# Performance work log

Measured on AMD Instinct MI355X. Metric: run time of the kernel, lower is better.

The kernel has to match this reference:

```python
import jax, jax.numpy as jnp
import numpy as np

N, C, T, H, W = 2, 512, 8, 28, 28
THW = T * H * W
BN_EPS = 1e-5


def conv1x1(x, Wt, b):
    # pointwise channel mixing, equivalent to 1x1 Conv2d/Conv3d on (N,C,T,H,W)
    return jnp.einsum('oc,ncthw->nothw', Wt, x) + b[None, :, None, None, None]


def setup_inputs() -> dict:
    key = jax.random.key(0)
    ks = jax.random.split(key, 8)
    s = 1.0 / np.sqrt(C)
    x = jax.random.normal(ks[0], (N, C, T, H, W), dtype=jnp.float32)
    mask = jax.random.uniform(ks[1], (N, C, T, H, W), dtype=jnp.float32)
    Wh = jax.random.normal(ks[2], (C, C), dtype=jnp.float32) * s
    Wg = jax.random.normal(ks[3], (C, C), dtype=jnp.float32) * s
    Wm = jax.random.normal(ks[4], (C, C), dtype=jnp.float32) * s
    Wz = jax.random.normal(ks[5], (C, C), dtype=jnp.float32) * s  # kaiming-like
    bh = jnp.zeros((C,), jnp.float32)
    bg = jnp.zeros((C,), jnp.float32)
    bm = jnp.zeros((C,), jnp.float32)
    bz = jnp.zeros((C,), jnp.float32)
    bn_w = jnp.ones((C,), jnp.float32)
    bn_b = jnp.zeros((C,), jnp.float32)
    gamma = jnp.float32(1.0)  # self.gamma (undefined in source __init__); learnable scalar
    return dict(x=x, mask=mask, Wh=Wh, bh=bh, Wg=Wg, bg=bg, Wm=Wm, bm=bm,
                Wz=Wz, bz=bz, bn_w=bn_w, bn_b=bn_b, gamma=gamma)


def reference(x, mask, Wh, bh, Wg, bg, Wm, bm, Wz, bz, bn_w, bn_b, gamma):
    n = x.shape[0]
    # proj_f = h(x) reshaped (N, THW, C); proj_g = g(x) (N, C, THW)
    ph_x = conv1x1(x, Wh, bh).reshape(n, C, THW)
    pg = conv1x1(x, Wg, bg).reshape(n, C, THW)
    # energy[n,t,s] = sum_c ph_x[n,c,t] * pg[n,c,s]  -> (N, THW, THW)
    energy = jnp.einsum('nct,ncs->nts', ph_x, pg)
    attention = jax.nn.softmax(energy, axis=-1)
    # proj_h uses self.h on mask (faithful to source)
    ph_m = conv1x1(mask, Wh, bh).reshape(n, C, THW)
    # bmm(proj_h, attention^T): [n,c,t] = sum_s ph_m[n,c,s] * attention[n,t,s]
    mask_energy = jnp.einsum('ncs,nts->nct', ph_m, attention)
    mask_atten = jax.nn.softmax(mask_energy, axis=-1)  # softmax over THW
    pm = conv1x1(x, Wm, bm)
    out = pm * mask_atten.reshape(n, C, T, H, W)
    # W_z: 1x1 Conv3d + BatchNorm3d (training-mode batch stats, weight=1, bias=0)
    wy = conv1x1(x, Wz, bz)
    mu = jnp.mean(wy, axis=(0, 2, 3, 4), keepdims=True)
    var = jnp.var(wy, axis=(0, 2, 3, 4), keepdims=True)
    wy = (wy - mu) * jax.lax.rsqrt(var + BN_EPS)
    wy = wy * bn_w[None, :, None, None, None] + bn_b[None, :, None, None, None]
    return gamma * out + wy
```

## Files before the change

kernel.cpp:

```cpp
#include <hip/hip_runtime.h>
#include <hip/hip_bf16.h>
#include <math.h>

#define NN 2
#define CC 512
#define PP 6272
#define TCHMAX 1664
#define NCHK 4
#define NJT 49
#define EM 64.0f
static const size_t PPC = (size_t)PP * CC;
static const size_t NCP = (size_t)NN * PPC;

typedef unsigned short ushortT;
typedef __attribute__((ext_vector_type(8))) short short8;
typedef __attribute__((ext_vector_type(4))) float f32x4;

#define WAITV(N) asm volatile("s_waitcnt vmcnt(" #N ")" ::: "memory")
#define BAR() __builtin_amdgcn_s_barrier()

__device__ __forceinline__ ushortT f2bf(float f) {
  __hip_bfloat16 h = __float2bfloat16(f);
  return *reinterpret_cast<ushortT*>(&h);
}
__device__ __forceinline__ float bf2f(ushortT u) {
  return __uint_as_float(((unsigned)u) << 16);
}

__device__ __forceinline__ void ld_g2l(const void* g, void* l) {
  __builtin_amdgcn_global_load_lds(
      (const __attribute__((address_space(1))) void*)g,
      (__attribute__((address_space(3))) void*)l, 16, 0, 0);
}

__device__ __forceinline__ int xcd_remap(int orig, int nwg) {
  const int q = nwg >> 3, r = nwg & 7;
  const int x = orig & 7, lo = orig >> 3;
  return (x < r) ? x * (q + 1) + lo : r * (q + 1) + (x - r) * q + lo;
}


__global__ __launch_bounds__(256) void k_prep(const float* __restrict__ x,
                                              const float* __restrict__ mask,
                                              const float* __restrict__ W0,
                                              const float* __restrict__ W1,
                                              const float* __restrict__ W2,
                                              const float* __restrict__ W3,
                                              ushortT* __restrict__ Wbf,
                                              ushortT* __restrict__ xT,
                                              ushortT* __restrict__ maskT) {
  __shared__ float T[32][33];
  const int tid = threadIdx.x;
  int b = blockIdx.x;
  if (b < 1024) {
    const int by = b >> 8, bx = b & 255;
    const float* src = (by == 0) ? W0 : (by == 1) ? W1 : (by == 2) ? W2 : W3;
    const int i = (bx * 256 + tid) * 4;
    float4 v = *(const float4*)&src[i];
    ushort4 o;
    o.x = f2bf(v.x); o.y = f2bf(v.y); o.z = f2bf(v.z); o.w = f2bf(v.w);
    *(ushort4*)&Wbf[(size_t)by * CC * CC + i] = o;
    return;
  }
  b -= 1024;
  const int bx = b % 196;
  const int by = (b / 196) & 15;
  const int zz = b / (196 * 16);
  const float* in = (zz < 2) ? x : mask;
  ushortT* out = (zz < 2) ? xT : maskT;
  const int p0 = bx * 32, c0 = by * 32;
  const int tx = tid & 31, ty = tid >> 5;
  const size_t nbi = (size_t)(zz & 1) * PPC;
#pragma unroll
  for (int i = 0; i < 4; ++i)
    T[ty + i * 8][tx] = in[nbi + (size_t)(c0 + ty + i * 8) * PP + p0 + tx];
  __syncthreads();
#pragma unroll
  for (int i = 0; i < 4; ++i) {
    int r = ty + i * 8;
    out[nbi + (size_t)(p0 + r) * CC + c0 + tx] = f2bf(T[tx][r]);
  }
}

__global__ __launch_bounds__(256, 2) void k_convs(
    const ushortT* __restrict__ xT, const ushortT* __restrict__ maskT,
    const ushortT* __restrict__ Whbf, const ushortT* __restrict__ Wgbf,
    const ushortT* __restrict__ Wmbf, const ushortT* __restrict__ Wzbf,
    const float* __restrict__ bh, const float* __restrict__ bg,
    const float* __restrict__ bm, const float* __restrict__ bz,
    ushortT* __restrict__ phxT, ushortT* __restrict__ pgT,
    ushortT* __restrict__ phmB, ushortT* __restrict__ pmB,
    ushortT* __restrict__ wzb) {
  __shared__ __align__(16) ushortT smem[36864];
  const int tid = threadIdx.x;
  const int l = tid & 63, w = tid >> 6;
  const int orig = blockIdx.x;
  const int wgid = (orig & 7) * 147 + (orig >> 3);
  const int zq = wgid / 196;
  const int within = wgid % 196;
  const int ctile = within & 3;
  const int ptile = within >> 2;
  const int wA = (w & 1) * 64, wB = (w >> 1) * 64;
  const int lr = l & 15, lk = l >> 4;
  const int r4 = (l >> 4) * 4;
  const int srow = l >> 2;
  const int sg8 = ((l & 3) ^ ((l >> 3) & 3)) * 8;
  const int rg16 = (lk ^ ((lr >> 1) & 3)) * 16;

  int offL[4], offR[4];
#pragma unroll
  for (int t = 0; t < 4; ++t) {
    offL[t] = (wA + t * 16 + lr) * 64 + rg16;
    offR[t] = (wB + t * 16 + lr) * 64 + rg16;
  }

  auto stage = [&](const ushortT* src, ushortT* dst) {
#pragma unroll
    for (int i = 0; i < 2; ++i)
      ld_g2l(src + (size_t)(w * 32 + i * 16 + srow) * CC + sg8,
             (char*)dst + (w * 2 + i) * 1024);
  };
  auto ldf = [&](const ushortT* base, const int* off, short8* f) {
#pragma unroll
    for (int t = 0; t < 4; ++t)
      f[t] = *(const short8*)((const char*)base + off[t]);
  };

  ushortT* Ca = smem;          ushortT* Na = smem + 4096;  ushortT* Za = smem + 8192;
  ushortT* Cb = smem + 12288;  ushortT* Nb = smem + 16384; ushortT* Zb = smem + 20480;
  ushortT* Cc = smem + 24576;  ushortT* Nc = smem + 28672; ushortT* Zc = smem + 32768;

  if (zq < 2) {
    const int zb = zq;
    const int p0 = ptile * 128, c0 = ctile * 128;
    const ushortT* Ax = xT + (size_t)zb * PPC + (size_t)p0 * CC;
    const ushortT* Bw1 = Whbf + (size_t)c0 * CC;
    const ushortT* Bw2 = Wgbf + (size_t)c0 * CC;
    ushortT* o1 = phxT + (size_t)zb * PPC;
    ushortT* o2 = pgT + (size_t)zb * PPC;
    f32x4 a1[4][4] = {}, a2[4][4] = {};
    stage(Ax, Ca); stage(Bw1, Cb); stage(Bw2, Cc);
    stage(Ax + 32, Na); stage(Bw1 + 32, Nb); stage(Bw2 + 32, Nc);
    WAITV(6); BAR();
    for (int t = 0; t < 16; ++t) {
      if (t < 14) {
        const int k = (t + 2) * 32;
        stage(Ax + k, Za); stage(Bw1 + k, Zb); stage(Bw2 + k, Zc);
      }
      short8 fp[4], fw[4];
      ldf(Ca, offL, fp);
      ldf(Cb, offR, fw);
      __builtin_amdgcn_s_setprio(1);
#pragma unroll
      for (int ss = 0; ss < 4; ++ss)
#pragma unroll
        for (int tt = 0; tt < 4; ++tt)
          a1[ss][tt] = __builtin_amdgcn_mfma_f32_16x16x32_bf16(fw[ss], fp[tt], a1[ss][tt], 0, 0, 0);
      __builtin_amdgcn_s_setprio(0);
      ldf(Cc, offR, fw);
      __builtin_amdgcn_s_setprio(1);
#pragma unroll
      for (int ss = 0; ss < 4; ++ss)
#pragma unroll
        for (int tt = 0; tt < 4; ++tt)
          a2[ss][tt] = __builtin_amdgcn_mfma_f32_16x16x32_bf16(fw[ss], fp[tt], a2[ss][tt], 0, 0, 0);
      __builtin_amdgcn_s_setprio(0);
      if (t < 14) { WAITV(6); } else { WAITV(0); }
      BAR();
      ushortT* tp;
      tp = Ca; Ca = Na; Na = Za; Za = tp;
      tp = Cb; Cb = Nb; Nb = Zb; Zb = tp;
      tp = Cc; Cc = Nc; Nc = Zc; Zc = tp;
    }
#pragma unroll
    for (int tt = 0; tt < 4; ++tt) {
      const size_t prow = (size_t)(p0 + wA + tt * 16 + lr) * CC;
#pragma unroll
      for (int ss = 0; ss < 4; ++ss) {
        const int co = c0 + wB + ss * 16 + r4;
        float4 b1v = *(const float4*)&bh[co];
        float4 b2v = *(const float4*)&bg[co];
        ushort4 v1, v2;
        v1.x = f2bf(a1[ss][tt][0] + b1v.x);
        v1.y = f2bf(a1[ss][tt][1] + b1v.y);
        v1.z = f2bf(a1[ss][tt][2] + b1v.z);
        v1.w = f2bf(a1[ss][tt][3] + b1v.w);
        v2.x = f2bf(a2[ss][tt][0] + b2v.x);
        v2.y = f2bf(a2[ss][tt][1] + b2v.y);
        v2.z = f2bf(a2[ss][tt][2] + b2v.z);
        v2.w = f2bf(a2[ss][tt][3] + b2v.w);
        *(ushort4*)&o1[prow + co] = v1;
        *(ushort4*)&o2[prow + co] = v2;
      }
    }
  } else if (zq < 4) {
    const int zb = zq - 2;
    const int s0 = ptile * 128, c0 = ctile * 128;
    const ushortT* Am = maskT + (size_t)zb * PPC + (size_t)s0 * CC;
    const ushortT* Bw = Whbf + (size_t)c0 * CC;
    ushortT* o = phmB + (size_t)zb * PPC;
    f32x4 a[4][4] = {};
    stage(Am, Ca); stage(Bw, Cb);
    stage(Am + 32, Na); stage(Bw + 32, Nb);
    WAITV(4); BAR();
    for (int t = 0; t < 16; ++t) {
      if (t < 14) {
        const int k = (t + 2) * 32;
        stage(Am + k, Za); stage(Bw + k, Zb);
      }
      short8 fs[4], fc[4];
      ldf(Ca, offL, fs);
      ldf(Cb, offR, fc);
      __builtin_amdgcn_s_setprio(1);
#pragma unroll
      for (int ss = 0; ss < 4; ++ss)
#pragma unroll
        for (int tt = 0; tt < 4; ++tt)
          a[ss][tt] = __builtin_amdgcn_mfma_f32_16x16x32_bf16(fs[ss], fc[tt], a[ss][tt], 0, 0, 0);
      __builtin_amdgcn_s_setprio(0);
      if (t < 14) { WAITV(4); } else { WAITV(0); }
      BAR();
      ushortT* tp;
      tp = Ca; Ca = Na; Na = Za; Za = tp;
      tp = Cb; Cb = Nb; Nb = Zb; Zb = tp;
    }
#pragma unroll
    for (int tt = 0; tt < 4; ++tt) {
      const int c = c0 + wB + tt * 16 + lr;
      const float bi = bh[c];
      const size_t crow = (size_t)c * PP;
#pragma unroll
      for (int ss = 0; ss < 4; ++ss) {
        ushort4 v;
        v.x = f2bf(a[ss][tt][0] + bi);
        v.y = f2bf(a[ss][tt][1] + bi);
        v.z = f2bf(a[ss][tt][2] + bi);
        v.w = f2bf(a[ss][tt][3] + bi);
        *(ushort4*)&o[crow + s0 + wA + ss * 16 + r4] = v;
      }
    }
  } else {
    const int zb = zq - 4;
    const int p0 = ptile * 128, c0 = ctile * 128;
    const ushortT* Ax = xT + (size_t)zb * PPC + (size_t)p0 * CC;
    const ushortT* Bw1 = Wmbf + (size_t)c0 * CC;
    const ushortT* Bw2 = Wzbf + (size_t)c0 * CC;
    ushortT* o1 = pmB + (size_t)zb * PPC;
    ushortT* o2 = wzb + (size_t)zb * PPC;
    f32x4 a1[4][4] = {}, a2[4][4] = {};
    stage(Ax, Ca); stage(Bw1, Cb); stage(Bw2, Cc);
    stage(Ax + 32, Na); stage(Bw1 + 32, Nb); stage(Bw2 + 32, Nc);
    WAITV(6); BAR();
    for (int t = 0; t < 16; ++t) {
      if (t < 14) {
        const int k = (t + 2) * 32;
        stage(Ax + k, Za); stage(Bw1 + k, Zb); stage(Bw2 + k, Zc);
      }
      short8 fx[4], fw[4];
      ldf(Ca, offL, fx);
      ldf(Cb, offR, fw);
      __builtin_amdgcn_s_setprio(1);
#pragma unroll
      for (int ss = 0; ss < 4; ++ss)
#pragma unroll
        for (int tt = 0; tt < 4; ++tt)
          a1[ss][tt] = __builtin_amdgcn_mfma_f32_16x16x32_bf16(fx[ss], fw[tt], a1[ss][tt], 0, 0, 0);
      __builtin_amdgcn_s_setprio(0);
      ldf(Cc, offR, fw);
      __builtin_amdgcn_s_setprio(1);
#pragma unroll
      for (int ss = 0; ss < 4; ++ss)
#pragma unroll
        for (int tt = 0; tt < 4; ++tt)
          a2[ss][tt] = __builtin_amdgcn_mfma_f32_16x16x32_bf16(fx[ss], fw[tt], a2[ss][tt], 0, 0, 0);
      __builtin_amdgcn_s_setprio(0);
      if (t < 14) { WAITV(6); } else { WAITV(0); }
      BAR();
      ushortT* tp;
      tp = Ca; Ca = Na; Na = Za; Za = tp;
      tp = Cb; Cb = Nb; Nb = Zb; Zb = tp;
      tp = Cc; Cc = Nc; Nc = Zc; Zc = tp;
    }
#pragma unroll
    for (int tt = 0; tt < 4; ++tt) {
      const int c = c0 + wB + tt * 16 + lr;
      const float b1v = bm[c], b2v = bz[c];
      const size_t crow = (size_t)c * PP;
#pragma unroll
      for (int ss = 0; ss < 4; ++ss) {
        const size_t off = crow + p0 + wA + ss * 16 + r4;
        ushort4 v1, v2;
        v1.x = f2bf(a1[ss][tt][0] + b1v);
        v1.y = f2bf(a1[ss][tt][1] + b1v);
        v1.z = f2bf(a1[ss][tt][2] + b1v);
        v1.w = f2bf(a1[ss][tt][3] + b1v);
        v2.x = f2bf(a2[ss][tt][0] + b2v);
        v2.y = f2bf(a2[ss][tt][1] + b2v);
        v2.z = f2bf(a2[ss][tt][2] + b2v);
        v2.w = f2bf(a2[ss][tt][3] + b2v);
        *(ushort4*)&o1[off] = v1;
        *(ushort4*)&o2[off] = v2;
      }
    }
  }
}

__global__ __launch_bounds__(256, 3) void k_energy(const ushortT* __restrict__ phxT,
                                                   const ushortT* __restrict__ pgT,
                                                   ushortT* __restrict__ Ech,
                                                   float* __restrict__ Estat,
                                                   int tbase) {
  __shared__ __align__(16) ushortT smem[24576];
  __shared__ float Ss[128][2];
  const int tid = threadIdx.x;
  const int l = tid & 63, w = tid >> 6;
  const int tiles = gridDim.y;
  const int orig = blockIdx.x + NJT * (blockIdx.y + tiles * blockIdx.z);
  const int wgid = xcd_remap(orig, NJT * tiles * NN);
  const int it = wgid % tiles;
  const int jt = (wgid / tiles) % NJT;
  const int z = wgid / (tiles * NJT);
  const int j0 = jt * 128;
  const int i0 = it * 128;
  const ushortT* Arow = phxT + (size_t)z * PPC + (size_t)(tbase + i0) * CC;
  const ushortT* Brow = pgT + (size_t)z * PPC + (size_t)j0 * CC;
  ushortT* out = Ech + (size_t)z * TCHMAX * PP;
  const int wi = (w & 1) * 64, wj = (w >> 1) * 64;
  const int lr = l & 15, lk = l >> 4;
  const int r4 = (l >> 4) * 4;
  const int srow = l >> 2;
  const int sg8 = ((l & 3) ^ ((l >> 3) & 3)) * 8;
  const int rg16 = (lk ^ ((lr >> 1) & 3)) * 16;

  int offA[4], offB[4];
#pragma unroll
  for (int t = 0; t < 4; ++t) {
    offA[t] = (wi + t * 16 + lr) * 64 + rg16;
    offB[t] = (wj + t * 16 + lr) * 64 + rg16;
  }
  auto stage = [&](const ushortT* src, ushortT* dst) {
#pragma unroll
    for (int i = 0; i < 2; ++i)
      ld_g2l(src + (size_t)(w * 32 + i * 16 + srow) * CC + sg8,
             (char*)dst + (w * 2 + i) * 1024);
  };

  ushortT* Ac = smem;          ushortT* An = smem + 4096;  ushortT* Az = smem + 8192;
  ushortT* Bc = smem + 12288;  ushortT* Bn = smem + 16384; ushortT* Bz = smem + 20480;

  f32x4 acc[4][4] = {};

  stage(Arow, Ac); stage(Brow, Bc);
  stage(Arow + 32, An); stage(Brow + 32, Bn);
  WAITV(4); BAR();
  for (int t = 0; t < 16; ++t) {
    if (t < 14) {
      const int k = (t + 2) * 32;
      stage(Arow + k, Az); stage(Brow + k, Bz);
    }
    short8 af[4], bfv[4];
#pragma unroll
    for (int tt = 0; tt < 4; ++tt)
      af[tt] = *(const short8*)((const char*)Ac + offA[tt]);
#pragma unroll
    for (int ss = 0; ss < 4; ++ss)
      bfv[ss] = *(const short8*)((const char*)Bc + offB[ss]);
    __builtin_amdgcn_s_setprio(1);
#pragma unroll
    for (int ss = 0; ss < 4; ++ss)
#pragma unroll
      for (int tt = 0; tt < 4; ++tt)
        acc[ss][tt] = __builtin_amdgcn_mfma_f32_16x16x32_bf16(bfv[ss], af[tt], acc[ss][tt], 0, 0, 0);
    __builtin_amdgcn_s_setprio(0);
    if (t < 14) { WAITV(4); } else { WAITV(0); }
    BAR();
    ushortT* tp;
    tp = Ac; Ac = An; An = Az; Az = tp;
    tp = Bc; Bc = Bn; Bn = Bz; Bz = tp;
  }
#pragma unroll
  for (int tt = 0; tt < 4; ++tt) {
    const int trow = i0 + wi + tt * 16 + lr;
    ushortT* orow = out + (size_t)trow * PP + j0;
    float sx = 0.f;
#pragma unroll
    for (int ss = 0; ss < 4; ++ss) {
      float u0 = __expf(acc[ss][tt][0] - EM);
      float u1 = __expf(acc[ss][tt][1] - EM);
      float u2 = __expf(acc[ss][tt][2] - EM);
      float u3 = __expf(acc[ss][tt][3] - EM);
      sx += (u0 + u1) + (u2 + u3);
      ushort4 v;
      v.x = f2bf(u0); v.y = f2bf(u1); v.z = f2bf(u2); v.w = f2bf(u3);
      *(ushort4*)&orow[wj + ss * 16 + r4] = v;
    }
    sx += __shfl_xor(sx, 16);
    sx += __shfl_xor(sx, 32);
    if (l < 16) Ss[wi + tt * 16 + l][w >> 1] = sx;
  }
  __syncthreads();
  if (tid < 128) {
    Estat[((size_t)z * TCHMAX + i0 + tid) * NJT + jt] = Ss[tid][0] + Ss[tid][1];
  }
}

__global__ __launch_bounds__(256) void k_zcomb(const float* __restrict__ Estat,
                                               float* __restrict__ rowZ, int rows) {
  const int r = blockIdx.x * 256 + threadIdx.x;
  if (r >= NN * rows) return;
  const int z = r / rows, tl = r % rows;
  const float* p = Estat + ((size_t)z * TCHMAX + tl) * NJT;
  float s = 0.f;
#pragma unroll
  for (int j = 0; j < NJT; ++j) s += p[j];
  rowZ[z * TCHMAX + tl] = 1.0f / s;
}

template <int KSPT>
__global__ __launch_bounds__(256, 4) void k_me(const ushortT* __restrict__ phmB,
                                               const ushortT* __restrict__ Ech,
                                               ushortT* __restrict__ mePart) {
  __shared__ __align__(16) ushortT smem[18432];
  const int tid = threadIdx.x;
  const int l = tid & 63, w = tid >> 6;
  const int gx = gridDim.x;
  const int orig = blockIdx.x + gx * (blockIdx.y + 4 * blockIdx.z);
  const int nwg = gx * 4 * (NN * KSPT);
  const int wgid = (orig & 7) * (nwg >> 3) + (orig >> 3);
  const int cb = wgid & 3;
  const int tl = (wgid >> 2) % gx;
  const int bz = (wgid >> 2) / gx;
  const int tl0 = tl * 64;
  const int c0 = cb * 128;
  const int z = bz / KSPT, ks = bz % KSPT;
  const ushortT* Arow = phmB + (size_t)z * PPC + (size_t)c0 * PP;
  const ushortT* Brow = Ech + (size_t)z * TCHMAX * PP + (size_t)tl0 * PP;
  const int wc = (w & 1) * 64, wt = (w >> 1) * 32;
  const int lr = l & 15, lk = l >> 4;
  const int r4 = (l >> 4) * 4;
  const int srow = l >> 2;
  const int sg8 = ((l & 3) ^ ((l >> 3) & 3)) * 8;
  const int rg16 = (lk ^ ((lr >> 1) & 3)) * 16;

  int offA[4], offB[2];
#pragma unroll
  for (int t = 0; t < 4; ++t) offA[t] = (wc + t * 16 + lr) * 64 + rg16;
#pragma unroll
  for (int t = 0; t < 2; ++t) offB[t] = (wt + t * 16 + lr) * 64 + rg16;

  auto stA = [&](const ushortT* src, ushortT* dst) {
#pragma unroll
    for (int i = 0; i < 2; ++i)
      ld_g2l(src + (size_t)(w * 32 + i * 16 + srow) * PP + sg8,
             (char*)dst + (w * 2 + i) * 1024);
  };
  auto stB = [&](const ushortT* src, ushortT* dst) {
    ld_g2l(src + (size_t)(w * 16 + srow) * PP + sg8, (char*)dst + w * 1024);
  };

  ushortT* Ac = smem;          ushortT* An = smem + 4096;  ushortT* Az = smem + 8192;
  ushortT* Bc = smem + 12288;  ushortT* Bn = smem + 14336; ushortT* Bz = smem + 16384;

  f32x4 acc[2][4] = {};

  const int sBeg = ((ks * 98) / KSPT) * 64;
  const int sEnd = (((ks + 1) * 98) / KSPT) * 64;
  const int NT = (sEnd - sBeg) >> 5;

  stA(Arow + sBeg, Ac); stB(Brow + sBeg, Bc);
  stA(Arow + sBeg + 32, An); stB(Brow + sBeg + 32, Bn);
  WAITV(3); BAR();
  for (int t = 0; t < NT; ++t) {
    if (t + 2 < NT) {
      const int k = sBeg + (t + 2) * 32;
      stA(Arow + k, Az); stB(Brow + k, Bz);
    }
    short8 af[4], bfv[2];
#pragma unroll
    for (int ct = 0; ct < 4; ++ct)
      af[ct] = *(const short8*)((const char*)Ac + offA[ct]);
#pragma unroll
    for (int tt = 0; tt < 2; ++tt)
      bfv[tt] = *(const short8*)((const char*)Bc + offB[tt]);
    __builtin_amdgcn_s_setprio(1);
#pragma unroll
    for (int tt = 0; tt < 2; ++tt)
#pragma unroll
      for (int ct = 0; ct < 4; ++ct)
        acc[tt][ct] = __builtin_amdgcn_mfma_f32_16x16x32_bf16(bfv[tt], af[ct], acc[tt][ct], 0, 0, 0);
    __builtin_amdgcn_s_setprio(0);
    if (t + 2 < NT) { WAITV(3); } else { WAITV(0); }
    BAR();
    ushortT* tp;
    tp = Ac; Ac = An; An = Az; Az = tp;
    tp = Bc; Bc = Bn; Bn = Bz; Bz = tp;
  }
  ushortT* out = mePart + ((size_t)(ks * NN + z) * CC) * TCHMAX;
#pragma unroll
  for (int ct = 0; ct < 4; ++ct) {
    const size_t crow = (size_t)(c0 + wc + ct * 16 + lr) * TCHMAX + tl0;
#pragma unroll
    for (int tt = 0; tt < 2; ++tt) {
      ushort4 v;
      v.x = f2bf(acc[tt][ct][0]);
      v.y = f2bf(acc[tt][ct][1]);
      v.z = f2bf(acc[tt][ct][2]);
      v.w = f2bf(acc[tt][ct][3]);
      *(ushort4*)&out[crow + wt + tt * 16 + r4] = v;
    }
  }
}

template <int KSPT>
__global__ __launch_bounds__(256) void k_meadd(const ushortT* __restrict__ mePart,
                                               const float* __restrict__ rowZ,
                                               ushortT* __restrict__ meb,
                                               int tbase, int rows) {
  const int idx = (blockIdx.x * 256 + threadIdx.x) * 4;
  const int tl = idx % rows;
  const int c = (idx / rows) % CC;
  const int z = idx / (rows * CC);
  float s0 = 0.f, s1 = 0.f, s2 = 0.f, s3 = 0.f;
#pragma unroll
  for (int ks = 0; ks < KSPT; ++ks) {
    const size_t o = ((size_t)(ks * NN + z) * CC + c) * TCHMAX + tl;
    ushort4 a = *(const ushort4*)&mePart[o];
    s0 += bf2f(a.x); s1 += bf2f(a.y); s2 += bf2f(a.z); s3 += bf2f(a.w);
  }
  const float4 rz = *(const float4*)&rowZ[z * TCHMAX + tl];
  ushort4 v;
  v.x = f2bf(s0 * rz.x); v.y = f2bf(s1 * rz.y);
  v.z = f2bf(s2 * rz.z); v.w = f2bf(s3 * rz.w);
  *(ushort4*)&meb[((size_t)z * CC + c) * PP + tbase + tl] = v;
}

__global__ __launch_bounds__(256) void k_stats(const ushortT* __restrict__ me,
                                               const ushortT* __restrict__ wz,
                                               float* __restrict__ m2,
                                               float* __restrict__ Z2,
                                               float* __restrict__ mu,
                                               float* __restrict__ rinv) {
  __shared__ float red[256];
  __shared__ float rq[256];
  const int tid = threadIdx.x;
  const int NCH = PP / 8;
  if ((int)blockIdx.x < NN * CC) {
    const ushortT* row = me + (size_t)blockIdx.x * PP;
    float m = -INFINITY;
    for (int i = tid; i < NCH; i += 256) {
      short8 v = *(const short8*)&row[i * 8];
#pragma unroll
      for (int j = 0; j < 8; ++j) m = fmaxf(m, bf2f((ushortT)v[j]));
    }
    red[tid] = m;
    __syncthreads();
    for (int s = 128; s > 0; s >>= 1) {
      if (tid < s) red[tid] = fmaxf(red[tid], red[tid + s]);
      __syncthreads();
    }
    m = red[0];
    __syncthreads();
    float zz = 0.f;
    for (int i = tid; i < NCH; i += 256) {
      short8 v = *(const short8*)&row[i * 8];
#pragma unroll
      for (int j = 0; j < 8; ++j) zz += __expf(bf2f((ushortT)v[j]) - m);
    }
    red[tid] = zz;
    __syncthreads();
    for (int s = 128; s > 0; s >>= 1) {
      if (tid < s) red[tid] += red[tid + s];
      __syncthreads();
    }
    if (tid == 0) { m2[blockIdx.x] = m; Z2[blockIdx.x] = red[0]; }
  } else {
    const int c = blockIdx.x - NN * CC;
    float s = 0.f, q = 0.f;
    for (int n = 0; n < NN; ++n) {
      const ushortT* rowp = wz + (size_t)n * CC * PP + (size_t)c * PP;
      for (int i = tid; i < NCH; i += 256) {
        short8 v = *(const short8*)&rowp[i * 8];
#pragma unroll
        for (int j = 0; j < 8; ++j) {
          float f = bf2f((ushortT)v[j]);
          s += f;
          q += f * f;
        }
      }
    }
    red[tid] = s; rq[tid] = q;
    __syncthreads();
    for (int st = 128; st > 0; st >>= 1) {
      if (tid < st) { red[tid] += red[tid + st]; rq[tid] += rq[tid + st]; }
      __syncthreads();
    }
    if (tid == 0) {
      const float inv_n = 1.0f / (float)(NN * PP);
      float mean = red[0] * inv_n;
      float var = rq[0] * inv_n - mean * mean;
      mu[c] = mean;
      rinv[c] = rsqrtf(var + 1e-5f);
    }
  }
}

__global__ __launch_bounds__(256) void k_final(const ushortT* __restrict__ pmB,
                                               const ushortT* __restrict__ me,
                                               const ushortT* __restrict__ wz,
                                               const float* __restrict__ m2,
                                               const float* __restrict__ Z2,
                                               const float* __restrict__ mu,
                                               const float* __restrict__ rinv,
                                               const float* __restrict__ bnw,
                                               const float* __restrict__ bnb,
                                               const float* __restrict__ gamma,
                                               float* __restrict__ out) {
  const int e4 = blockIdx.x * 256 + threadIdx.x;
  const size_t e = (size_t)e4 * 4;
  const int nc = (int)(e / PP);
  const int c = nc & (CC - 1);
  const float m = m2[nc];
  const float rz = 1.0f / Z2[nc];
  const float mub = mu[c];
  const float ri = rinv[c] * bnw[c];
  const float bb = bnb[c];
  const float g = gamma[0];
  ushort4 pv = *(const ushort4*)&pmB[e];
  ushort4 mev = *(const ushort4*)&me[e];
  ushort4 wzv = *(const ushort4*)&wz[e];
  float4 o;
  o.x = g * bf2f(pv.x) * (__expf(bf2f(mev.x) - m) * rz) + (bf2f(wzv.x) - mub) * ri + bb;
  o.y = g * bf2f(pv.y) * (__expf(bf2f(mev.y) - m) * rz) + (bf2f(wzv.y) - mub) * ri + bb;
  o.z = g * bf2f(pv.z) * (__expf(bf2f(mev.z) - m) * rz) + (bf2f(wzv.z) - mub) * ri + bb;
  o.w = g * bf2f(pv.w) * (__expf(bf2f(mev.w) - m) * rz) + (bf2f(wzv.w) - mub) * ri + bb;
  *(float4*)&out[e] = o;
}

extern "C" void kernel_launch(void* const* d_in, const int* in_sizes, int n_in,
                              void* d_out, int out_size, void* d_ws, size_t ws_size,
                              hipStream_t stream) {
  (void)in_sizes; (void)n_in; (void)out_size;
  const float* x    = (const float*)d_in[0];
  const float* mask = (const float*)d_in[1];
  const float* Wh   = (const float*)d_in[2];
  const float* bh   = (const float*)d_in[3];
  const float* Wg   = (const float*)d_in[4];
  const float* bg   = (const float*)d_in[5];
  const float* Wm   = (const float*)d_in[6];
  const float* bm   = (const float*)d_in[7];
  const float* Wz   = (const float*)d_in[8];
  const float* bz   = (const float*)d_in[9];
  const float* bnw  = (const float*)d_in[10];
  const float* bnb  = (const float*)d_in[11];
  const float* gam  = (const float*)d_in[12];

  ushortT* wzb  = (ushortT*)d_ws;
  ushortT* meb  = wzb + NCP;
  ushortT* pmB  = meb + NCP;
  ushortT* phxT = pmB + NCP;
  ushortT* pgT  = phxT + NCP;
  ushortT* phmB = pgT + NCP;
  ushortT* Wbf  = phmB + NCP;
  ushortT* Whbf = Wbf;
  ushortT* Wgbf = Wbf + 1 * CC * CC;
  ushortT* Wmbf = Wbf + 2 * CC * CC;
  ushortT* Wzbf = Wbf + 3 * CC * CC;
  float* m2    = (float*)(Wbf + 4 * CC * CC);
  float* Z2    = m2 + NN * CC;
  float* mu    = Z2 + NN * CC;
  float* rin   = mu + CC;
  float* Estat = rin + CC;
  float* rowZ  = Estat + (size_t)NN * TCHMAX * NJT;
  float* region = rowZ + (size_t)NN * TCHMAX + 16;
  ushortT* xT    = (ushortT*)region;
  ushortT* maskT = xT + NCP;
  ushortT* Ech    = (ushortT*)region;
  ushortT* mePart = Ech + (size_t)NN * TCHMAX * PP;

  const size_t regionOffB = (size_t)((char*)region - (char*)d_ws);
  const size_t need8 = regionOffB +
      ((size_t)NN * TCHMAX * PP + 8ull * NN * CC * TCHMAX) * 2;
  const bool k8 = ws_size >= need8;

  k_prep<<<1024 + 196 * 16 * 4, 256, 0, stream>>>(x, mask, Wh, Wg, Wm, Wz,
                                                  Wbf, xT, maskT);

  k_convs<<<1176, 256, 0, stream>>>(xT, maskT, Whbf, Wgbf, Wmbf, Wzbf,
                                    bh, bg, bm, bz, phxT, pgT, phmB, pmB, wzb);

  static const int chunkTiles[NCHK] = {13, 12, 12, 12};
  int tbase = 0;
  for (int ch = 0; ch < NCHK; ++ch) {
    const int tiles = chunkTiles[ch];
    const int rows = tiles * 128;
    dim3 gE(NJT, tiles, NN);
    k_energy<<<gE, 256, 0, stream>>>(phxT, pgT, Ech, Estat, tbase);
    k_zcomb<<<(NN * rows + 255) / 256, 256, 0, stream>>>(Estat, rowZ, rows);
    if (k8) {
      dim3 gM(rows / 64, CC / 128, NN * 8);
      k_me<8><<<gM, 256, 0, stream>>>(phmB, Ech, mePart);
      k_meadd<8><<<NN * CC * rows / 1024, 256, 0, stream>>>(mePart, rowZ, meb,
                                                            tbase, rows);
    } else {
      dim3 gM(rows / 64, CC / 128, NN * 4);
      k_me<4><<<gM, 256, 0, stream>>>(phmB, Ech, mePart);
      k_meadd<4><<<NN * CC * rows / 1024, 256, 0, stream>>>(mePart, rowZ, meb,
                                                            tbase, rows);
    }
    tbase += rows;
  }

  k_stats<<<NN * CC + CC, 256, 0, stream>>>(meb, wzb, m2, Z2, mu, rin);
  const int total4 = (int)(NCP / 4);
  k_final<<<total4 / 256, 256, 0, stream>>>(pmB, meb, wzb, m2, Z2, mu, rin,
                                            bnw, bnb, gam, (float*)d_out);
}
```

Before: 537.9 us.

## Fold zcomb into k_me and overlap meadd with next chunk's energy

The per-chunk row-normalizer kernel (zcomb) becomes extra tail blocks of the mask-energy GEMM kernel. The partial-sum reduction (meadd) of each chunk now runs as extra blocks inside the next chunk's energy GEMM launch, and only the last chunk keeps a standalone meadd. This cuts the number of kernel launches and the serialization gaps between small kernels, and lets the bandwidth-bound reduction overlap compute-bound GEMM tiles. In exchange, the grids become 1D with extra blocks, and the mask-energy kernel's launch bound drops from 4 to 3 waves per SIMD, which may lower its occupancy.

```diff
diff --git a/kernel.cpp b/kernel.cpp
--- a/kernel.cpp
+++ b/kernel.cpp
@@ -305,24 +305,47 @@
   }
 }
 
-__global__ __launch_bounds__(256, 3) void k_energy(const ushortT* __restrict__ phxT,
-                                                   const ushortT* __restrict__ pgT,
-                                                   ushortT* __restrict__ Ech,
-                                                   float* __restrict__ Estat,
-                                                   int tbase) {
+template <int KSPT>
+__global__ __launch_bounds__(256, 3) void k_eadd(
+    const ushortT* __restrict__ phxT, const ushortT* __restrict__ pgT,
+    ushortT* __restrict__ Ech, float* __restrict__ Estat,
+    int tbaseE, int tilesE, int nE,
+    const ushortT* __restrict__ mePart, const float* __restrict__ rowZ,
+    ushortT* __restrict__ meb, int tbaseM, int rowsM) {
   __shared__ __align__(16) ushortT smem[24576];
   __shared__ float Ss[128][2];
   const int tid = threadIdx.x;
+  if ((int)blockIdx.x >= nE) {
+    const int total4 = NN * CC * rowsM / 4;
+    for (int e4 = ((int)blockIdx.x - nE) * 256 + tid; e4 < total4; e4 += 65536) {
+      const int idx = e4 * 4;
+      const int tl = idx % rowsM;
+      const int c = (idx / rowsM) % CC;
+      const int z = idx / (rowsM * CC);
+      float s0 = 0.f, s1 = 0.f, s2 = 0.f, s3 = 0.f;
+#pragma unroll
+      for (int ks = 0; ks < KSPT; ++ks) {
+        const size_t o = ((size_t)(ks * NN + z) * CC + c) * TCHMAX + tl;
+        ushort4 a = *(const ushort4*)&mePart[o];
+        s0 += bf2f(a.x); s1 += bf2f(a.y); s2 += bf2f(a.z); s3 += bf2f(a.w);
+      }
+      const float4 rz = *(const float4*)&rowZ[z * TCHMAX + tl];
+      ushort4 v;
+      v.x = f2bf(s0 * rz.x); v.y = f2bf(s1 * rz.y);
+      v.z = f2bf(s2 * rz.z); v.w = f2bf(s3 * rz.w);
+      *(ushort4*)&meb[((size_t)z * CC + c) * PP + tbaseM + tl] = v;
+    }
+    return;
+  }
   const int l = tid & 63, w = tid >> 6;
-  const int tiles = gridDim.y;
-  const int orig = blockIdx.x + NJT * (blockIdx.y + tiles * blockIdx.z);
-  const int wgid = xcd_remap(orig, NJT * tiles * NN);
-  const int it = wgid % tiles;
-  const int jt = (wgid / tiles) % NJT;
-  const int z = wgid / (tiles * NJT);
+  const int orig = blockIdx.x;
+  const int wgid = xcd_remap(orig, NJT * tilesE * NN);
+  const int it = wgid % tilesE;
+  const int jt = (wgid / tilesE) % NJT;
+  const int z = wgid / (tilesE * NJT);
   const int j0 = jt * 128;
   const int i0 = it * 128;
-  const ushortT* Arow = phxT + (size_t)z * PPC + (size_t)(tbase + i0) * CC;
+  const ushortT* Arow = phxT + (size_t)z * PPC + (size_t)(tbaseE + i0) * CC;
   const ushortT* Brow = pgT + (size_t)z * PPC + (size_t)j0 * CC;
   ushortT* out = Ech + (size_t)z * TCHMAX * PP;
   const int wi = (w & 1) * 64, wj = (w >> 1) * 64;
@@ -404,32 +427,31 @@
   }
 }
 
-__global__ __launch_bounds__(256) void k_zcomb(const float* __restrict__ Estat,
-                                               float* __restrict__ rowZ, int rows) {
-  const int r = blockIdx.x * 256 + threadIdx.x;
-  if (r >= NN * rows) return;
-  const int z = r / rows, tl = r % rows;
-  const float* p = Estat + ((size_t)z * TCHMAX + tl) * NJT;
-  float s = 0.f;
-#pragma unroll
-  for (int j = 0; j < NJT; ++j) s += p[j];
-  rowZ[z * TCHMAX + tl] = 1.0f / s;
-}
-
 template <int KSPT>
-__global__ __launch_bounds__(256, 4) void k_me(const ushortT* __restrict__ phmB,
-                                               const ushortT* __restrict__ Ech,
-                                               ushortT* __restrict__ mePart) {
+__global__ __launch_bounds__(256, 3) void k_mezc(
+    const ushortT* __restrict__ phmB, const ushortT* __restrict__ Ech,
+    ushortT* __restrict__ mePart, int gxM, int nM,
+    const float* __restrict__ Estat, float* __restrict__ rowZ, int rows) {
   __shared__ __align__(16) ushortT smem[18432];
   const int tid = threadIdx.x;
+  if ((int)blockIdx.x >= nM) {
+    const int r = ((int)blockIdx.x - nM) * 256 + tid;
+    if (r >= NN * rows) return;
+    const int z = r / rows, tl = r % rows;
+    const float* p = Estat + ((size_t)z * TCHMAX + tl) * NJT;
+    float s = 0.f;
+#pragma unroll
+    for (int j = 0; j < NJT; ++j) s += p[j];
+    rowZ[z * TCHMAX + tl] = 1.0f / s;
+    return;
+  }
   const int l = tid & 63, w = tid >> 6;
-  const int gx = gridDim.x;
-  const int orig = blockIdx.x + gx * (blockIdx.y + 4 * blockIdx.z);
-  const int nwg = gx * 4 * (NN * KSPT);
+  const int orig = blockIdx.x;
+  const int nwg = gxM * 4 * (NN * KSPT);
   const int wgid = (orig & 7) * (nwg >> 3) + (orig >> 3);
   const int cb = wgid & 3;
-  const int tl = (wgid >> 2) % gx;
-  const int bz = (wgid >> 2) / gx;
+  const int tl = (wgid >> 2) % gxM;
+  const int bz = (wgid >> 2) / gxM;
   const int tl0 = tl * 64;
   const int c0 = cb * 128;
   const int z = bz / KSPT, ks = bz % KSPT;
@@ -689,25 +711,51 @@
                                     bh, bg, bm, bz, phxT, pgT, phmB, pmB, wzb);
 
   static const int chunkTiles[NCHK] = {13, 12, 12, 12};
-  int tbase = 0;
+  int tb[NCHK];
+  {
+    int acc = 0;
+    for (int ch = 0; ch < NCHK; ++ch) { tb[ch] = acc; acc += chunkTiles[ch] * 128; }
+  }
+  const int KSPv = k8 ? 8 : 4;
+  {
+    const int nE = NJT * chunkTiles[0] * NN;
+    if (k8)
+      k_eadd<8><<<nE, 256, 0, stream>>>(phxT, pgT, Ech, Estat, tb[0],
+                                        chunkTiles[0], nE, mePart, rowZ, meb, 0, 0);
+    else
+      k_eadd<4><<<nE, 256, 0, stream>>>(phxT, pgT, Ech, Estat, tb[0],
+                                        chunkTiles[0], nE, mePart, rowZ, meb, 0, 0);
+  }
   for (int ch = 0; ch < NCHK; ++ch) {
-    const int tiles = chunkTiles[ch];
-    const int rows = tiles * 128;
-    dim3 gE(NJT, tiles, NN);
-    k_energy<<<gE, 256, 0, stream>>>(phxT, pgT, Ech, Estat, tbase);
-    k_zcomb<<<(NN * rows + 255) / 256, 256, 0, stream>>>(Estat, rowZ, rows);
-    if (k8) {
-      dim3 gM(rows / 64, CC / 128, NN * 8);
-      k_me<8><<<gM, 256, 0, stream>>>(phmB, Ech, mePart);
-      k_meadd<8><<<NN * CC * rows / 1024, 256, 0, stream>>>(mePart, rowZ, meb,
-                                                            tbase, rows);
+    const int rows = chunkTiles[ch] * 128;
+    const int gxM = rows / 64;
+    const int nM = gxM * 4 * NN * KSPv;
+    const int zcB = (NN * rows + 255) / 256;
+    if (k8)
+      k_mezc<8><<<nM + zcB, 256, 0, stream>>>(phmB, Ech, mePart, gxM, nM,
+                                              Estat, rowZ, rows);
+    else
+      k_mezc<4><<<nM + zcB, 256, 0, stream>>>(phmB, Ech, mePart, gxM, nM,
+                                              Estat, rowZ, rows);
+    if (ch < NCHK - 1) {
+      const int tilesN = chunkTiles[ch + 1];
+      const int nE = NJT * tilesN * NN;
+      if (k8)
+        k_eadd<8><<<nE + 256, 256, 0, stream>>>(phxT, pgT, Ech, Estat, tb[ch + 1],
+                                                tilesN, nE, mePart, rowZ, meb,
+                                                tb[ch], rows);
+      else
+        k_eadd<4><<<nE + 256, 256, 0, stream>>>(phxT, pgT, Ech, Estat, tb[ch + 1],
+                                                tilesN, nE, mePart, rowZ, meb,
+                                                tb[ch], rows);
     } else {
-      dim3 gM(rows / 64, CC / 128, NN * 4);
-      k_me<4><<<gM, 256, 0, stream>>>(phmB, Ech, mePart);
-      k_meadd<4><<<NN * CC * rows / 1024, 256, 0, stream>>>(mePart, rowZ, meb,
-                                                            tbase, rows);
-    }
-    tbase += rows;
+      if (k8)
+        k_meadd<8><<<NN * CC * rows / 1024, 256, 0, stream>>>(mePart, rowZ, meb,
+                                                              tb[ch], rows);
+      else
+        k_meadd<4><<<NN * CC * rows / 1024, 256, 0, stream>>>(mePart, rowZ, meb,
+                                                              tb[ch], rows);
+    }
   }
 
   k_stats<<<NN * CC + CC, 256, 0, stream>>>(meb, wzb, m2, Z2, mu, rin);
```

After: 515.1 us. 4.2% less time.
